# Kernel tuning notes

Hardware: AMD Instinct MI355X
Metric: run time of the kernel (lower is better)

Reference implementation:

```python
import jax, jax.numpy as jnp
import numpy as np
from jax import lax

K = 7  # kernel_size
PAD = K // 2


def _feature_difference(t):
    # t: [B, C, H, W] -> normalized census-style local differences [B, K*K, H, W]
    intensity = t.mean(axis=1, keepdims=True)  # [B,1,H,W]
    # Equivalent to conv2d with the identity (eye) kernel in the torch module:
    # channel k gathers the neighbor at offset (k//K, k%K) with zero padding.
    patches = lax.conv_general_dilated_patches(
        intensity, filter_shape=(K, K), window_strides=(1, 1),
        padding=[(PAD, PAD), (PAD, PAD)])  # [B, K*K, H, W]
    local_diff = patches - intensity
    return local_diff / jnp.sqrt(0.81 + local_diff * local_diff)


def setup_inputs() -> dict:
    key = jax.random.key(0)
    kx, ky = jax.random.split(key)
    B, C, H, W = 8, 3, 320, 1024
    x = jax.random.uniform(kx, (B, C, H, W), dtype=jnp.float32)
    y = jax.random.uniform(ky, (B, C, H, W), dtype=jnp.float32)
    return {"x": x, "y": y}


def reference(x, y):
    diff_x = _feature_difference(x)
    diff_y = _feature_difference(y)
    diff_total = diff_x - lax.stop_gradient(diff_y)  # .detach() on y branch
    d2 = diff_total * diff_total
    dist = (d2 / (0.1 + d2)).mean(axis=1, keepdims=True)  # [B,1,H,W]
    b, c, h, w = x.shape
    # valid-region mask: ones in the interior, zeros in the PAD-wide border
    mask = jnp.zeros((b, 1, h, w), dtype=x.dtype)
    mask = mask.at[:, :, PAD:h - PAD, PAD:w - PAD].set(1.0)
    return (dist * mask).mean()
```

## Files before the change

### kernel.cpp

```cpp
#include <hip/hip_runtime.h>

#define PAD 3
#define HH 320
#define WW 1024
#define BB 8
#define TH 32
#define TW 64
#define HALO_H (TH + 2*PAD)
#define HALO_W (TW + 2*PAD)
#define LDS_W  72
#define RPW 8

#define NIN ((HH - 2*PAD) * (WW - 2*PAD))
#define OUT_SCALE (1.0 / (49.0 * (double)BB * (double)HH * (double)WW))
#define C0 ((float)(48.0 * (double)BB * (double)NIN * OUT_SCALE))
#define NEG_SCALE ((float)(-0.1 * OUT_SCALE))

__global__ __launch_bounds__(256) void ternary_loss_kernel(
    const float* __restrict__ x, const float* __restrict__ y,
    float* __restrict__ out)
{
    __shared__ float sIx[HALO_H][LDS_W];
    __shared__ float sIy[HALO_H][LDS_W];
    __shared__ float wave_sums[4];

    const int tile_j = blockIdx.x * TW;
    const int tile_i = blockIdx.y * TH;
    const int b      = blockIdx.z;
    const int tx  = threadIdx.x;
    const int wv  = threadIdx.y;
    const int tid = wv * 64 + tx;

    const float* xb = x + (size_t)b * 3 * HH * WW;
    const float* yb = y + (size_t)b * 3 * HH * WW;

    for (int idx = tid; idx < HALO_H * HALO_W; idx += 256) {
        int r = idx / HALO_W;
        int c = idx - r * HALO_W;
        int gi = tile_i - PAD + r;
        int gj = tile_j - PAD + c;
        float vx = 0.0f, vy = 0.0f;
        if (gi >= 0 && gi < HH && gj >= 0 && gj < WW) {
            size_t o = (size_t)gi * WW + gj;
            vx = (xb[o] + xb[(size_t)HH * WW + o] + xb[2 * (size_t)HH * WW + o]) * (1.0f / 3.0f);
            vy = (yb[o] + yb[(size_t)HH * WW + o] + yb[2 * (size_t)HH * WW + o]) * (1.0f / 3.0f);
        }
        sIx[r][c] = vx;
        sIy[r][c] = vy;
    }
    __syncthreads();

    const int gj = tile_j + tx;
    float colOK[7];
    #pragma unroll
    for (int d = 0; d < 7; ++d) {
        int nj = gj + d - 3;
        colOK[d] = (nj >= PAD && nj < WW - PAD) ? 1.0f : 0.0f;
    }

    const int li0 = wv * RPW;

    float wx[4][7], wy[4][7];
    #pragma unroll
    for (int r = 0; r < 3; ++r) {
        #pragma unroll
        for (int d = 0; d < 7; ++d) {
            wx[r][d] = sIx[li0 + 3 + r][tx + d];
            wy[r][d] = sIy[li0 + 3 + r][tx + d];
        }
    }

    float acc = 0.0f;

    #pragma unroll 1
    for (int io = 0; io < RPW / 4; ++io) {
        #pragma unroll
        for (int iu = 0; iu < 4; ++iu) {
            const int li = li0 + io * 4 + iu;
            const int gi = tile_i + li;
            const int snew = (iu + 3) & 3;
            #pragma unroll
            for (int d = 0; d < 7; ++d) {
                wx[snew][d] = sIx[li + 6][tx + d];
                wy[snew][d] = sIy[li + 6][tx + d];
            }

            float rin[4];
            #pragma unroll
            for (int di = 0; di < 4; ++di) {
                int ni = gi + di;
                rin[di] = (ni >= PAD && ni < HH - PAD) ? 1.0f : 0.0f;
            }
            const float mc = rin[0] * colOK[3];

            const float cx = wx[iu & 3][3];
            const float cy = wy[iu & 3][3];

            #pragma unroll
            for (int di = 0; di <= 3; ++di) {
                const int s = (iu + di) & 3;
                #pragma unroll
                for (int dj = -3; dj <= 3; ++dj) {
                    if (di == 0 && dj <= 0) continue;
                    float nx = wx[s][dj + 3];
                    float ny = wy[s][dj + 3];
                    float dx = nx - cx;
                    float gx = dx * __builtin_amdgcn_rsqf(fmaf(dx, dx, 0.81f));
                    float dy = ny - cy;
                    float gy = dy * __builtin_amdgcn_rsqf(fmaf(dy, dy, 0.81f));
                    float t  = gx - gy;
                    float denom = fmaf(t, t, 0.1f);
                    float r = __builtin_amdgcn_rcpf(denom);
                    float w = fmaf(rin[di], colOK[dj + 3], mc);
                    acc = fmaf(w, r, acc);
                }
            }
        }
    }

    #pragma unroll
    for (int off = 32; off > 0; off >>= 1)
        acc += __shfl_down(acc, off, 64);
    if (tx == 0) wave_sums[wv] = acc;
    __syncthreads();
    if (tid == 0) {
        float total = (wave_sums[0] + wave_sums[1] + wave_sums[2] + wave_sums[3]) * NEG_SCALE;
        if (blockIdx.x == 0 && blockIdx.y == 0 && blockIdx.z == 0)
            total += C0;
        atomicAdd(out, total);
    }
}

extern "C" void kernel_launch(void* const* d_in, const int* in_sizes, int n_in,
                              void* d_out, int out_size, void* d_ws, size_t ws_size,
                              hipStream_t stream) {
    const float* x = (const float*)d_in[0];
    const float* y = (const float*)d_in[1];
    float* out = (float*)d_out;

    hipMemsetAsync(out, 0, sizeof(float), stream);

    dim3 grid(WW / TW, HH / TH, BB);
    dim3 block(64, 4, 1);
    ternary_loss_kernel<<<grid, block, 0, stream>>>(x, y, out);
}
```

Baseline: 127.0 us.

## Pack neighbor pairs into float2 math with fused rsq and shared reciprocal

Restructures the per-neighbor loss math so two neighbors are processed as packed float2 operations. The two rsqrt calls are merged into one rsqrt of the product, and the two reciprocals are combined into a single rcp over the product of denominators, which cuts transcendental instruction count. The halo load is vectorized to float4 global loads and LDS stores, with the tile shifted by one column for alignment. It also sets a launch-bounds occupancy hint and adds asm barriers to keep LDS loads in place. In exchange it adds packed multiplies and carries some risk of overflow or precision loss from combining the terms.

```diff
diff --git a/kernel.cpp b/kernel.cpp
--- a/kernel.cpp
+++ b/kernel.cpp
@@ -1,4 +1,7 @@
 #include <hip/hip_runtime.h>
+
+typedef float f32x2 __attribute__((ext_vector_type(2)));
+typedef float f32x4 __attribute__((ext_vector_type(4)));
 
 #define PAD 3
 #define HH 320
@@ -7,8 +10,9 @@
 #define TH 32
 #define TW 64
 #define HALO_H (TH + 2*PAD)
-#define HALO_W (TW + 2*PAD)
 #define LDS_W  72
+#define NF4    (LDS_W/4)
+#define NPOS   (HALO_H * NF4)
 #define RPW 8
 
 #define NIN ((HH - 2*PAD) * (WW - 2*PAD))
@@ -16,12 +20,41 @@
 #define C0 ((float)(48.0 * (double)BB * (double)NIN * OUT_SCALE))
 #define NEG_SCALE ((float)(-0.1 * OUT_SCALE))
 
-__global__ __launch_bounds__(256) void ternary_loss_kernel(
+#define KEEP(v) asm("" : "+v"(v))
+
+__device__ __forceinline__ f32x2 mk2(float a, float b) { f32x2 r; r.x = a; r.y = b; return r; }
+__device__ __forceinline__ f32x2 sp2(float a)          { f32x2 r; r.x = a; r.y = a; return r; }
+__device__ __forceinline__ f32x2 fma2(f32x2 a, f32x2 b, f32x2 c) {
+    return __builtin_elementwise_fma(a, b, c);
+}
+
+__device__ __forceinline__ void pair2(f32x2 nx, f32x2 ny, f32x2 cx2, f32x2 cy2,
+                                      f32x2 w2, float& acc)
+{
+    f32x2 dx  = nx - cx2;
+    f32x2 dy  = ny - cy2;
+    f32x2 dx2 = dx * dx;
+    f32x2 dy2 = dy * dy;
+    f32x2 ax  = dx2 + sp2(0.81f);
+    f32x2 ay  = dy2 + sp2(0.81f);
+    f32x2 P   = ax * ay;
+    f32x2 s   = mk2(__builtin_amdgcn_rsqf(P.x), __builtin_amdgcn_rsqf(P.y));
+    f32x2 A   = fma2(dx2, ay, dy2 * ax);
+    f32x2 h   = dx * dy;
+    f32x2 inner = fma2(s, A, h * sp2(-2.0f));
+    f32x2 t2  = s * inner;
+    f32x2 den = t2 + sp2(0.1f);
+    float ip    = __builtin_amdgcn_rcpf(den.x * den.y);
+    float cross = fmaf(w2.x, den.y, w2.y * den.x);
+    acc = fmaf(ip, cross, acc);
+}
+
+__global__ __launch_bounds__(256, 4) void ternary_loss_kernel(
     const float* __restrict__ x, const float* __restrict__ y,
     float* __restrict__ out)
 {
-    __shared__ float sIx[HALO_H][LDS_W];
-    __shared__ float sIy[HALO_H][LDS_W];
+    __shared__ __align__(16) float sIx[HALO_H][LDS_W];
+    __shared__ __align__(16) float sIy[HALO_H][LDS_W];
     __shared__ float wave_sums[4];
 
     const int tile_j = blockIdx.x * TW;
@@ -31,32 +64,45 @@
     const int wv  = threadIdx.y;
     const int tid = wv * 64 + tx;
 
-    const float* xb = x + (size_t)b * 3 * HH * WW;
-    const float* yb = y + (size_t)b * 3 * HH * WW;
+    const size_t PLANE = (size_t)HH * WW;
+    const float* xb = x + (size_t)b * 3 * PLANE;
+    const float* yb = y + (size_t)b * 3 * PLANE;
 
-    for (int idx = tid; idx < HALO_H * HALO_W; idx += 256) {
-        int r = idx / HALO_W;
-        int c = idx - r * HALO_W;
-        int gi = tile_i - PAD + r;
-        int gj = tile_j - PAD + c;
-        float vx = 0.0f, vy = 0.0f;
-        if (gi >= 0 && gi < HH && gj >= 0 && gj < WW) {
-            size_t o = (size_t)gi * WW + gj;
-            vx = (xb[o] + xb[(size_t)HH * WW + o] + xb[2 * (size_t)HH * WW + o]) * (1.0f / 3.0f);
-            vy = (yb[o] + yb[(size_t)HH * WW + o] + yb[2 * (size_t)HH * WW + o]) * (1.0f / 3.0f);
+    for (int p = tid; p < NPOS; p += 256) {
+        int r  = p / NF4;
+        int c4 = p - r * NF4;
+        int gi  = tile_i - PAD + r;
+        int gj0 = tile_j - 4 + 4 * c4;
+        f32x4 vx = {0.0f, 0.0f, 0.0f, 0.0f};
+        f32x4 vy = {0.0f, 0.0f, 0.0f, 0.0f};
+        if ((unsigned)gi < (unsigned)HH && (unsigned)gj0 < (unsigned)WW) {
+            const float* px = xb + (size_t)gi * WW + gj0;
+            f32x4 a0 = *(const f32x4*)(px);
+            f32x4 a1 = *(const f32x4*)(px + PLANE);
+            f32x4 a2 = *(const f32x4*)(px + 2 * PLANE);
+            vx = (a0 + a1 + a2) * (1.0f / 3.0f);
+            const float* py = yb + (size_t)gi * WW + gj0;
+            f32x4 b0 = *(const f32x4*)(py);
+            f32x4 b1 = *(const f32x4*)(py + PLANE);
+            f32x4 b2 = *(const f32x4*)(py + 2 * PLANE);
+            vy = (b0 + b1 + b2) * (1.0f / 3.0f);
         }
-        sIx[r][c] = vx;
-        sIy[r][c] = vy;
+        *(f32x4*)&sIx[r][4 * c4] = vx;
+        *(f32x4*)&sIy[r][4 * c4] = vy;
     }
     __syncthreads();
 
     const int gj = tile_j + tx;
-    float colOK[7];
+    float cO[7];
     #pragma unroll
     for (int d = 0; d < 7; ++d) {
         int nj = gj + d - 3;
-        colOK[d] = (nj >= PAD && nj < WW - PAD) ? 1.0f : 0.0f;
+        cO[d] = (nj >= PAD && nj < WW - PAD) ? 1.0f : 0.0f;
     }
+    const f32x2 cP0  = mk2(cO[0], cO[1]);
+    const f32x2 cP1  = mk2(cO[2], cO[3]);
+    const f32x2 cP2  = mk2(cO[4], cO[5]);
+    const f32x2 cP3  = sp2(cO[6]);
 
     const int li0 = wv * RPW;
 
@@ -65,8 +111,8 @@
     for (int r = 0; r < 3; ++r) {
         #pragma unroll
         for (int d = 0; d < 7; ++d) {
-            wx[r][d] = sIx[li0 + 3 + r][tx + d];
-            wy[r][d] = sIy[li0 + 3 + r][tx + d];
+            float a = sIx[li0 + 3 + r][tx + 1 + d]; KEEP(a); wx[r][d] = a;
+            float c = sIy[li0 + 3 + r][tx + 1 + d]; KEEP(c); wy[r][d] = c;
         }
     }
 
@@ -81,8 +127,8 @@
             const int snew = (iu + 3) & 3;
             #pragma unroll
             for (int d = 0; d < 7; ++d) {
-                wx[snew][d] = sIx[li + 6][tx + d];
-                wy[snew][d] = sIy[li + 6][tx + d];
+                float a = sIx[li + 6][tx + 1 + d]; KEEP(a); wx[snew][d] = a;
+                float c = sIy[li + 6][tx + 1 + d]; KEEP(c); wy[snew][d] = c;
             }
 
             float rin[4];
@@ -91,29 +137,36 @@
                 int ni = gi + di;
                 rin[di] = (ni >= PAD && ni < HH - PAD) ? 1.0f : 0.0f;
             }
-            const float mc = rin[0] * colOK[3];
+            const float mc  = rin[0] * cO[3];
+            const f32x2 mc2 = sp2(mc);
 
-            const float cx = wx[iu & 3][3];
-            const float cy = wy[iu & 3][3];
+            const int s0 = iu & 3;
+            const f32x2 cx2 = sp2(wx[s0][3]);
+            const f32x2 cy2 = sp2(wy[s0][3]);
+
+            pair2(mk2(wx[s0][4], wx[s0][5]), mk2(wy[s0][4], wy[s0][5]),
+                  cx2, cy2, fma2(sp2(rin[0]), cP2, mc2), acc);
 
             #pragma unroll
-            for (int di = 0; di <= 3; ++di) {
+            for (int di = 1; di <= 3; ++di) {
                 const int s = (iu + di) & 3;
-                #pragma unroll
-                for (int dj = -3; dj <= 3; ++dj) {
-                    if (di == 0 && dj <= 0) continue;
-                    float nx = wx[s][dj + 3];
-                    float ny = wy[s][dj + 3];
-                    float dx = nx - cx;
-                    float gx = dx * __builtin_amdgcn_rsqf(fmaf(dx, dx, 0.81f));
-                    float dy = ny - cy;
-                    float gy = dy * __builtin_amdgcn_rsqf(fmaf(dy, dy, 0.81f));
-                    float t  = gx - gy;
-                    float denom = fmaf(t, t, 0.1f);
-                    float r = __builtin_amdgcn_rcpf(denom);
-                    float w = fmaf(rin[di], colOK[dj + 3], mc);
-                    acc = fmaf(w, r, acc);
-                }
+                const f32x2 rin2 = sp2(rin[di]);
+                pair2(mk2(wx[s][0], wx[s][1]), mk2(wy[s][0], wy[s][1]),
+                      cx2, cy2, fma2(rin2, cP0, mc2), acc);
+                pair2(mk2(wx[s][2], wx[s][3]), mk2(wy[s][2], wy[s][3]),
+                      cx2, cy2, fma2(rin2, cP1, mc2), acc);
+                pair2(mk2(wx[s][4], wx[s][5]), mk2(wy[s][4], wy[s][5]),
+                      cx2, cy2, fma2(rin2, cP2, mc2), acc);
+            }
+
+            {
+                const int s1 = (iu + 1) & 3;
+                const int s2 = (iu + 2) & 3;
+                const int s3 = (iu + 3) & 3;
+                pair2(mk2(wx[s0][6], wx[s1][6]), mk2(wy[s0][6], wy[s1][6]),
+                      cx2, cy2, fma2(mk2(rin[0], rin[1]), cP3, mc2), acc);
+                pair2(mk2(wx[s2][6], wx[s3][6]), mk2(wy[s2][6], wy[s3][6]),
+                      cx2, cy2, fma2(mk2(rin[2], rin[3]), cP3, mc2), acc);
             }
         }
     }
```

Measured after the change: 120.6 us. 1.05x faster.
